# Optimization experiments

Hardware: AMD Instinct MI355X
Metric: run time of the kernel (lower is better)

## Reference

```python
import jax, jax.numpy as jnp
import numpy as np

INPUT_DIM = 512
HIDDEN_DIM = 1024


def glorot_normal(key, shape):
    fan_in, fan_out = shape[0], shape[1]
    std = jnp.sqrt(2.0 / (fan_in + fan_out))
    return std * jax.random.normal(key, shape, dtype=jnp.float32)


def setup_inputs() -> dict:
    key = jax.random.key(0)
    k1, k2, k3 = jax.random.split(key, 3)
    b, t = 32, 1024
    H = HIDDEN_DIM + INPUT_DIM
    x_btd = jax.random.normal(k1, (b, t, INPUT_DIM), dtype=jnp.float32)
    input_paddings = jnp.zeros((b, t), dtype=jnp.float32)
    kernel = glorot_normal(k2, (H, 4 * HIDDEN_DIM))  # [H, 4h]
    bias = jnp.zeros((4 * HIDDEN_DIM,), dtype=jnp.float32)
    h_init = glorot_normal(k3, (1, HIDDEN_DIM))
    return {"x_btd": x_btd, "input_paddings": input_paddings,
            "kernel": kernel, "bias": bias, "h_init": h_init}


def lstm_step(carry, x_bd, kernel, bias):
    h_bh, c_bh = carry
    x_bH = jnp.concatenate([x_bd, h_bh], axis=-1)          # [b, d+h]
    gate_out = jnp.einsum('bH,Hh->bh', x_bH, kernel) + bias  # [b, 4h]
    f, i, o, g = jnp.split(gate_out, 4, axis=-1)
    c_new = jax.nn.sigmoid(f) * c_bh + jax.nn.sigmoid(i) * jnp.tanh(g)
    h_new = jax.nn.sigmoid(o) * jnp.tanh(c_new)
    return (h_new, c_new), h_new


def reference(x_btd, input_paddings, kernel, bias, h_init) -> jnp.ndarray:
    del input_paddings
    b = x_btd.shape[0]
    h0 = jnp.tile(h_init, (b, 1))                # [b, h]
    c0 = jnp.zeros((b, HIDDEN_DIM), dtype=x_btd.dtype)
    x_tbd = jnp.transpose(x_btd, (1, 0, 2))      # [t, b, d]

    def step(carry, x_bd):
        return lstm_step(carry, x_bd, kernel, bias)

    _, h_tbh = jax.lax.scan(step, (h0, c0), x_tbd)
    return jnp.transpose(h_tbh, (1, 0, 2))       # [b, t, h]
```

## Files before the change

kernel.cpp:

```cpp
#include <hip/hip_runtime.h>


#define T_STEPS 1024
#define BATCH   32
#define DIN     512
#define HID     1024
#define KTOT    1536
#define NBLK    128
#define REDSTR  36
#define REDW    (32*REDSTR)
#define NSLOT   8
#define FLAGSTR 16

typedef __attribute__((ext_vector_type(8))) short  short8;
typedef __attribute__((ext_vector_type(4))) float  floatx4;
typedef __attribute__((ext_vector_type(4))) int    intx4;
typedef __attribute__((ext_vector_type(4))) unsigned short ushort4_;

#define MFMA16(a,b,c) __builtin_amdgcn_mfma_f32_16x16x32_bf16(a, b, c, 0, 0, 0)

__device__ __forceinline__ unsigned short f2bf(float f) {
    unsigned u = __builtin_bit_cast(unsigned, f);
    u += 0x7FFFu + ((u >> 16) & 1u);
    return (unsigned short)(u >> 16);
}
__device__ __forceinline__ float sigf(float x) { return 1.f / (1.f + __expf(-x)); }
__device__ __forceinline__ float tanh_fast(float x) {
    float e = __expf(2.f * x);
    return 1.f - 2.f / (e + 1.f);
}

__device__ __forceinline__ floatx4 coh_load16(const void* p) {
    floatx4 v;
    asm volatile("global_load_dwordx4 %0, %1, off sc1" : "=v"(v) : "v"(p));
    return v;
}
__device__ __forceinline__ intx4 coh_load16i(const void* p) {
    intx4 v;
    asm volatile("global_load_dwordx4 %0, %1, off sc1\n\ts_waitcnt vmcnt(0)"
                 : "=v"(v) : "v"(p) : "memory");
    return v;
}
__device__ __forceinline__ void coh_store16(void* p, short8 v) {
    asm volatile("global_store_dwordx4 %0, %1, off sc1" :: "v"(p), "v"(v) : "memory");
}
__device__ __forceinline__ void coh_store4(void* p, int v) {
    asm volatile("global_store_dword %0, %1, off sc1" :: "v"(p), "v"(v) : "memory");
}
__device__ __forceinline__ void wait_vm0() {
    asm volatile("s_waitcnt vmcnt(0)" ::: "memory");
}

__global__ __launch_bounds__(256) void prep_wt(const float* __restrict__ kern,
                                               unsigned short* __restrict__ wt) {
    __shared__ unsigned short tile[64][72];
    const int c0 = (blockIdx.x & 63) * 64;
    const int k0 = (blockIdx.x >> 6) * 64;
    const int cl = threadIdx.x & 63;
    const int kg = threadIdx.x >> 6;
    #pragma unroll
    for (int i = 0; i < 16; ++i) {
        int kl = kg * 16 + i;
        tile[cl][kl] = f2bf(kern[(k0 + kl) * 4096 + c0 + cl]);
    }
    __syncthreads();
    #pragma unroll
    for (int i = 0; i < 16; ++i) {
        int cc = kg * 16 + i;
        wt[(size_t)(c0 + cc) * KTOT + k0 + cl] = tile[cc][cl];
    }
}

__global__ __launch_bounds__(256) void prep_x(const float* __restrict__ x,
                                              unsigned short* __restrict__ xT) {
    const int row = blockIdx.x * 2 + (threadIdx.x >> 7);
    const int l   = threadIdx.x & 127;
    const int b = row >> 10, t = row & 1023;
    float4 v = ((const float4*)(x + (size_t)row * DIN))[l];
    ushort4_ o;
    o.x = f2bf(v.x); o.y = f2bf(v.y); o.z = f2bf(v.z); o.w = f2bf(v.w);
    *(ushort4_*)(xT + ((size_t)t * BATCH + b) * DIN + l * 4) = o;
}

__global__ __launch_bounds__(256) void init_h(const float* __restrict__ h_init,
                                              unsigned short* __restrict__ hbuf,
                                              int* __restrict__ flags) {
    if (blockIdx.x == 32) {
        for (int i = threadIdx.x; i < NBLK * FLAGSTR; i += 256) flags[i] = 0;
        return;
    }
    const int p0 = blockIdx.x * 4;
    const int u = threadIdx.x & 7;
    #pragma unroll
    for (int j = 0; j < 4; ++j) {
        const int p = p0 + j;
        hbuf[p * 256 + threadIdx.x] = f2bf(h_init[p * 8 + u]);
    }
}

__global__ __launch_bounds__(512, 2) void lstm_persist(
    const unsigned short* __restrict__ wt,
    const unsigned short* __restrict__ xT,
    unsigned short* __restrict__ hbuf,
    int* __restrict__ flags,
    const float* __restrict__ bias,
    float* __restrict__ out)
{
    __shared__ float red[NSLOT][REDW];
    __shared__ __align__(16) unsigned short hLDS[256];

    const int bk   = blockIdx.x;
    const int tid  = threadIdx.x;
    const int wave = tid >> 6;
    const int lane = tid & 63;
    const int lrow = lane & 15;
    const int kq   = lane >> 4;
    const bool isG = wave < 4;
    const int  sl  = wave & 3;

    short8 wb[8][2];
    if (isG) {
        #pragma unroll
        for (int i = 0; i < 4; ++i) {
            const int k = sl * 128 + i * 32 + kq * 8;
            #pragma unroll
            for (int c = 0; c < 2; ++c) {
                const int cl = lrow + c * 16;
                const int gcol = (cl >> 3) * HID + bk * 8 + (cl & 7);
                wb[i][c] = *(const short8*)(wt + (size_t)gcol * KTOT + k);
            }
        }
    } else {
        #pragma unroll
        for (int i = 0; i < 8; ++i) {
            const int k = 512 + sl * 256 + i * 32 + kq * 8;
            #pragma unroll
            for (int c = 0; c < 2; ++c) {
                const int cl = lrow + c * 16;
                const int gcol = (cl >> 3) * HID + bk * 8 + (cl & 7);
                wb[i][c] = *(const short8*)(wt + (size_t)gcol * KTOT + k);
            }
        }
    }

    const int pb = tid >> 3;
    const int pu = tid & 7;
    float bias_r[4];
    float c_state = 0.f;
    if (tid < 256) {
        #pragma unroll
        for (int g = 0; g < 4; ++g) bias_r[g] = bias[g * HID + bk * 8 + pu];
    }

    const int* myflag = flags + (sl * 32 + (lane & 31)) * FLAGSTR;

    floatx4 xa[4][2];

    {
        const floatx4 zero = {0.f, 0.f, 0.f, 0.f};
        floatx4 acc[2][2] = {{zero, zero}, {zero, zero}};
        if (isG) {
            const unsigned short* xb = xT;
            #pragma unroll
            for (int i = 0; i < 4; ++i) {
                const int k = sl * 128 + i * 32 + kq * 8;
                short8 a0 = *(const short8*)(xb + lrow * DIN + k);
                short8 a1 = *(const short8*)(xb + (lrow + 16) * DIN + k);
                acc[0][0] = MFMA16(a0, wb[i][0], acc[0][0]);
                acc[0][1] = MFMA16(a0, wb[i][1], acc[0][1]);
                acc[1][0] = MFMA16(a1, wb[i][0], acc[1][0]);
                acc[1][1] = MFMA16(a1, wb[i][1], acc[1][1]);
            }
            const unsigned short* xn = xT + (size_t)1 * (BATCH * DIN);
            #pragma unroll
            for (int i = 0; i < 4; ++i) {
                const int k = sl * 128 + i * 32 + kq * 8;
                xa[i][0] = *(const floatx4*)(xn + lrow * DIN + k);
                xa[i][1] = *(const floatx4*)(xn + (lrow + 16) * DIN + k);
            }
        } else {
            floatx4 ha[8][2];
            #pragma unroll
            for (int i = 0; i < 8; ++i) {
                const int p = sl * 32 + i * 4 + kq;
                ha[i][0] = coh_load16(hbuf + p * 256 + lrow * 8);
                ha[i][1] = coh_load16(hbuf + p * 256 + (lrow + 16) * 8);
            }
            wait_vm0();
            __builtin_amdgcn_sched_barrier(0);
            #pragma unroll
            for (int i = 0; i < 8; ++i) {
                short8 a0 = __builtin_bit_cast(short8, ha[i][0]);
                short8 a1 = __builtin_bit_cast(short8, ha[i][1]);
                acc[0][0] = MFMA16(a0, wb[i][0], acc[0][0]);
                acc[0][1] = MFMA16(a0, wb[i][1], acc[0][1]);
                acc[1][0] = MFMA16(a1, wb[i][0], acc[1][0]);
                acc[1][1] = MFMA16(a1, wb[i][1], acc[1][1]);
            }
        }
        #pragma unroll
        for (int mt = 0; mt < 2; ++mt)
            #pragma unroll
            for (int nt = 0; nt < 2; ++nt)
                #pragma unroll
                for (int r = 0; r < 4; ++r)
                    red[wave][(mt * 16 + kq * 4 + r) * REDSTR + nt * 16 + lrow]
                        = acc[mt][nt][r];
    }

    for (int t = 0; t < T_STEPS; ++t) {
        __syncthreads();

        if (tid < 256) {
            float gv[4];
            #pragma unroll
            for (int g = 0; g < 4; ++g) {
                float s = bias_r[g];
                #pragma unroll
                for (int w = 0; w < NSLOT; ++w)
                    s += red[w][pb * REDSTR + g * 8 + pu];
                gv[g] = s;
            }
            const float fg = sigf(gv[0]);
            const float ig = sigf(gv[1]);
            const float og = sigf(gv[2]);
            const float gg = tanh_fast(gv[3]);
            c_state = fg * c_state + ig * gg;
            const float hn = og * tanh_fast(c_state);

            if (t + 1 < T_STEPS) {
                hLDS[tid] = f2bf(hn);
                asm volatile("s_waitcnt lgkmcnt(0)" ::: "memory");
                if (lane < 8) {
                    short8 v = *(const short8*)(hLDS + wave * 64 + lane * 8);
                    coh_store16(hbuf + (size_t)((t + 1) & 1) * (NBLK * 256)
                                     + bk * 256 + (wave * 8 + lane) * 8, v);
                }
                wait_vm0();
                if (lane == 0)
                    coh_store4(flags + bk * FLAGSTR + wave, t + 1);
            }
            out[(size_t)pb * (T_STEPS * HID) + (size_t)t * HID + bk * 8 + pu] = hn;
        }

        if (t + 1 == T_STEPS) break;

        __syncthreads();

        const floatx4 zero = {0.f, 0.f, 0.f, 0.f};
        floatx4 acc[2][2] = {{zero, zero}, {zero, zero}};
        if (isG) {
            #pragma unroll
            for (int i = 0; i < 4; ++i) {
                short8 a0 = __builtin_bit_cast(short8, xa[i][0]);
                short8 a1 = __builtin_bit_cast(short8, xa[i][1]);
                acc[0][0] = MFMA16(a0, wb[i][0], acc[0][0]);
                acc[0][1] = MFMA16(a0, wb[i][1], acc[0][1]);
                acc[1][0] = MFMA16(a1, wb[i][0], acc[1][0]);
                acc[1][1] = MFMA16(a1, wb[i][1], acc[1][1]);
            }
            if (t + 2 < T_STEPS) {
                const unsigned short* xn = xT + (size_t)(t + 2) * (BATCH * DIN);
                #pragma unroll
                for (int i = 0; i < 4; ++i) {
                    const int k = sl * 128 + i * 32 + kq * 8;
                    xa[i][0] = *(const floatx4*)(xn + lrow * DIN + k);
                    xa[i][1] = *(const floatx4*)(xn + (lrow + 16) * DIN + k);
                }
            }
        } else {
            const int tgt = t + 1;
            while (true) {
                intx4 f = coh_load16i(myflag);
                if (f.x >= tgt && f.y >= tgt && f.z >= tgt && f.w >= tgt) break;
                __builtin_amdgcn_s_sleep(1);
            }
            const unsigned short* hb = hbuf + (size_t)((t + 1) & 1) * (NBLK * 256);
            floatx4 ha[8][2];
            #pragma unroll
            for (int i = 0; i < 8; ++i) {
                const int p = sl * 32 + i * 4 + kq;
                ha[i][0] = coh_load16(hb + p * 256 + lrow * 8);
                ha[i][1] = coh_load16(hb + p * 256 + (lrow + 16) * 8);
            }
            wait_vm0();
            __builtin_amdgcn_sched_barrier(0);
            #pragma unroll
            for (int i = 0; i < 8; ++i) {
                short8 a0 = __builtin_bit_cast(short8, ha[i][0]);
                short8 a1 = __builtin_bit_cast(short8, ha[i][1]);
                acc[0][0] = MFMA16(a0, wb[i][0], acc[0][0]);
                acc[0][1] = MFMA16(a0, wb[i][1], acc[0][1]);
                acc[1][0] = MFMA16(a1, wb[i][0], acc[1][0]);
                acc[1][1] = MFMA16(a1, wb[i][1], acc[1][1]);
            }
        }
        #pragma unroll
        for (int mt = 0; mt < 2; ++mt)
            #pragma unroll
            for (int nt = 0; nt < 2; ++nt)
                #pragma unroll
                for (int r = 0; r < 4; ++r)
                    red[wave][(mt * 16 + kq * 4 + r) * REDSTR + nt * 16 + lrow]
                        = acc[mt][nt][r];
    }
}

extern "C" void kernel_launch(void* const* d_in, const int* in_sizes, int n_in,
                              void* d_out, int out_size, void* d_ws, size_t ws_size,
                              hipStream_t stream) {
    (void)in_sizes; (void)n_in; (void)out_size;
    const float* x      = (const float*)d_in[0];
    const float* kern   = (const float*)d_in[2];
    const float* bias   = (const float*)d_in[3];
    const float* h_init = (const float*)d_in[4];
    float* out = (float*)d_out;

    char* ws = (char*)d_ws;
    unsigned short* wt    = (unsigned short*)(ws);
    unsigned short* xT    = (unsigned short*)(ws + 12582912);
    unsigned short* hbuf  = (unsigned short*)(ws + 12582912 + 33554432);
    int*            flags = (int*)(ws + 12582912 + 33554432 + 131072);
    (void)ws_size;

    prep_wt<<<dim3(64 * 24), dim3(256), 0, stream>>>(kern, wt);
    prep_x<<<dim3(BATCH * T_STEPS / 2), dim3(256), 0, stream>>>(x, xT);
    init_h<<<dim3(33), dim3(256), 0, stream>>>(h_init, hbuf, flags);

    void* args[] = { &wt, &xT, &hbuf, &flags, &bias, &out };
    hipLaunchCooperativeKernel((const void*)lstm_persist, dim3(NBLK), dim3(512),
                               args, 0, stream);
}
```

Before: 4.401 ms.

## Embed step-parity tag in fp32 hidden state to replace flag polling

The separate per-block flag array and its store-then-flag-store handshake are removed. Each hidden value is now written as fp32 with its low mantissa bit replaced by a step-parity tag, and consumers poll the data itself until every tag matches, then convert to bf16 with v_cvt_pk_bf16_f32. The x-projection MFMAs are also moved into the gate waves' post-activation phase so they overlap with the h polling, dropping one barrier-separated segment. The cost is doubled hidden-state traffic (fp32 instead of bf16), wider polling reads, and one mantissa bit of precision lost in h.

```diff
diff --git a/kernel.cpp b/kernel.cpp
--- a/kernel.cpp
+++ b/kernel.cpp
@@ -10,11 +10,11 @@
 #define REDSTR  36
 #define REDW    (32*REDSTR)
 #define NSLOT   8
-#define FLAGSTR 16
+#define HSLOT   (NBLK*256)
 
 typedef __attribute__((ext_vector_type(8))) short  short8;
 typedef __attribute__((ext_vector_type(4))) float  floatx4;
-typedef __attribute__((ext_vector_type(4))) int    intx4;
+typedef __attribute__((ext_vector_type(4))) unsigned int uintx4;
 typedef __attribute__((ext_vector_type(4))) unsigned short ushort4_;
 
 #define MFMA16(a,b,c) __builtin_amdgcn_mfma_f32_16x16x32_bf16(a, b, c, 0, 0, 0)
@@ -29,22 +29,18 @@
     float e = __expf(2.f * x);
     return 1.f - 2.f / (e + 1.f);
 }
-
-__device__ __forceinline__ floatx4 coh_load16(const void* p) {
+__device__ __forceinline__ unsigned cvt2(float a, float b) {
+    unsigned r;
+    asm("v_cvt_pk_bf16_f32 %0, %1, %2" : "=v"(r) : "v"(a), "v"(b));
+    return r;
+}
+
+__device__ __forceinline__ floatx4 coh_load16f(const void* p) {
     floatx4 v;
     asm volatile("global_load_dwordx4 %0, %1, off sc1" : "=v"(v) : "v"(p));
     return v;
 }
-__device__ __forceinline__ intx4 coh_load16i(const void* p) {
-    intx4 v;
-    asm volatile("global_load_dwordx4 %0, %1, off sc1\n\ts_waitcnt vmcnt(0)"
-                 : "=v"(v) : "v"(p) : "memory");
-    return v;
-}
-__device__ __forceinline__ void coh_store16(void* p, short8 v) {
-    asm volatile("global_store_dwordx4 %0, %1, off sc1" :: "v"(p), "v"(v) : "memory");
-}
-__device__ __forceinline__ void coh_store4(void* p, int v) {
+__device__ __forceinline__ void coh_store4u(void* p, unsigned v) {
     asm volatile("global_store_dword %0, %1, off sc1" :: "v"(p), "v"(v) : "memory");
 }
 __device__ __forceinline__ void wait_vm0() {
@@ -83,31 +79,26 @@
 }
 
 __global__ __launch_bounds__(256) void init_h(const float* __restrict__ h_init,
-                                              unsigned short* __restrict__ hbuf,
-                                              int* __restrict__ flags) {
-    if (blockIdx.x == 32) {
-        for (int i = threadIdx.x; i < NBLK * FLAGSTR; i += 256) flags[i] = 0;
-        return;
-    }
+                                              unsigned* __restrict__ hbuf_u) {
     const int p0 = blockIdx.x * 4;
     const int u = threadIdx.x & 7;
     #pragma unroll
     for (int j = 0; j < 4; ++j) {
         const int p = p0 + j;
-        hbuf[p * 256 + threadIdx.x] = f2bf(h_init[p * 8 + u]);
+        unsigned tv = __builtin_bit_cast(unsigned, h_init[p * 8 + u]) & ~1u;
+        hbuf_u[p * 256 + threadIdx.x] = tv;
+        hbuf_u[HSLOT + p * 256 + threadIdx.x] = 1u;
     }
 }
 
 __global__ __launch_bounds__(512, 2) void lstm_persist(
     const unsigned short* __restrict__ wt,
     const unsigned short* __restrict__ xT,
-    unsigned short* __restrict__ hbuf,
-    int* __restrict__ flags,
+    float* __restrict__ hbuf,
     const float* __restrict__ bias,
     float* __restrict__ out)
 {
     __shared__ float red[NSLOT][REDW];
-    __shared__ __align__(16) unsigned short hLDS[256];
 
     const int bk   = blockIdx.x;
     const int tid  = threadIdx.x;
@@ -118,6 +109,8 @@
     const bool isG = wave < 4;
     const int  sl  = wave & 3;
 
+    unsigned* hbuf_u = (unsigned*)hbuf;
+
     short8 wb[8][2];
     if (isG) {
         #pragma unroll
@@ -151,8 +144,6 @@
         #pragma unroll
         for (int g = 0; g < 4; ++g) bias_r[g] = bias[g * HID + bk * 8 + pu];
     }
-
-    const int* myflag = flags + (sl * 32 + (lane & 31)) * FLAGSTR;
 
     floatx4 xa[4][2];
 
@@ -179,23 +170,33 @@
                 xa[i][1] = *(const floatx4*)(xn + (lrow + 16) * DIN + k);
             }
         } else {
-            floatx4 ha[8][2];
+            floatx4 hf[8][2][2];
             #pragma unroll
             for (int i = 0; i < 8; ++i) {
                 const int p = sl * 32 + i * 4 + kq;
-                ha[i][0] = coh_load16(hbuf + p * 256 + lrow * 8);
-                ha[i][1] = coh_load16(hbuf + p * 256 + (lrow + 16) * 8);
+                #pragma unroll
+                for (int c = 0; c < 2; ++c) {
+                    const float* src = hbuf + p * 256 + (lrow + c * 16) * 8;
+                    hf[i][c][0] = coh_load16f(src);
+                    hf[i][c][1] = coh_load16f(src + 4);
+                }
             }
             wait_vm0();
             __builtin_amdgcn_sched_barrier(0);
             #pragma unroll
             for (int i = 0; i < 8; ++i) {
-                short8 a0 = __builtin_bit_cast(short8, ha[i][0]);
-                short8 a1 = __builtin_bit_cast(short8, ha[i][1]);
-                acc[0][0] = MFMA16(a0, wb[i][0], acc[0][0]);
-                acc[0][1] = MFMA16(a0, wb[i][1], acc[0][1]);
-                acc[1][0] = MFMA16(a1, wb[i][0], acc[1][0]);
-                acc[1][1] = MFMA16(a1, wb[i][1], acc[1][1]);
+                union { short8 s; unsigned u[4]; } wa[2];
+                #pragma unroll
+                for (int c = 0; c < 2; ++c) {
+                    wa[c].u[0] = cvt2(hf[i][c][0][0], hf[i][c][0][1]);
+                    wa[c].u[1] = cvt2(hf[i][c][0][2], hf[i][c][0][3]);
+                    wa[c].u[2] = cvt2(hf[i][c][1][0], hf[i][c][1][1]);
+                    wa[c].u[3] = cvt2(hf[i][c][1][2], hf[i][c][1][3]);
+                }
+                acc[0][0] = MFMA16(wa[0].s, wb[i][0], acc[0][0]);
+                acc[0][1] = MFMA16(wa[0].s, wb[i][1], acc[0][1]);
+                acc[1][0] = MFMA16(wa[1].s, wb[i][0], acc[1][0]);
+                acc[1][1] = MFMA16(wa[1].s, wb[i][1], acc[1][1]);
             }
         }
         #pragma unroll
@@ -210,6 +211,12 @@
 
     for (int t = 0; t < T_STEPS; ++t) {
         __syncthreads();
+
+        const unsigned tg = ((unsigned)(t + 1) >> 1) & 1u;
+        const size_t   so = (size_t)((t + 1) & 1) * HSLOT;
+
+        const floatx4 zero = {0.f, 0.f, 0.f, 0.f};
+        floatx4 acc[2][2] = {{zero, zero}, {zero, zero}};
 
         if (tid < 256) {
             float gv[4];
@@ -229,72 +236,81 @@
             const float hn = og * tanh_fast(c_state);
 
             if (t + 1 < T_STEPS) {
-                hLDS[tid] = f2bf(hn);
-                asm volatile("s_waitcnt lgkmcnt(0)" ::: "memory");
-                if (lane < 8) {
-                    short8 v = *(const short8*)(hLDS + wave * 64 + lane * 8);
-                    coh_store16(hbuf + (size_t)((t + 1) & 1) * (NBLK * 256)
-                                     + bk * 256 + (wave * 8 + lane) * 8, v);
+                unsigned hv = (__builtin_bit_cast(unsigned, hn) & ~1u) | tg;
+                coh_store4u(hbuf_u + so + bk * 256 + tid, hv);
+            }
+            out[(size_t)pb * (T_STEPS * HID) + (size_t)t * HID + bk * 8 + pu] = hn;
+
+            if (t + 1 < T_STEPS) {
+                #pragma unroll
+                for (int i = 0; i < 4; ++i) {
+                    short8 a0 = __builtin_bit_cast(short8, xa[i][0]);
+                    short8 a1 = __builtin_bit_cast(short8, xa[i][1]);
+                    acc[0][0] = MFMA16(a0, wb[i][0], acc[0][0]);
+                    acc[0][1] = MFMA16(a0, wb[i][1], acc[0][1]);
+                    acc[1][0] = MFMA16(a1, wb[i][0], acc[1][0]);
+                    acc[1][1] = MFMA16(a1, wb[i][1], acc[1][1]);
+                }
+                if (t + 2 < T_STEPS) {
+                    const unsigned short* xn = xT + (size_t)(t + 2) * (BATCH * DIN);
+                    #pragma unroll
+                    for (int i = 0; i < 4; ++i) {
+                        const int k = sl * 128 + i * 32 + kq * 8;
+                        xa[i][0] = *(const floatx4*)(xn + lrow * DIN + k);
+                        xa[i][1] = *(const floatx4*)(xn + (lrow + 16) * DIN + k);
+                    }
+                }
+            }
+        } else if (t + 1 < T_STEPS) {
+            const float* hb = hbuf + so;
+            floatx4 hf[8][2][2];
+            while (true) {
+                #pragma unroll
+                for (int i = 0; i < 8; ++i) {
+                    const int p = sl * 32 + i * 4 + kq;
+                    #pragma unroll
+                    for (int c = 0; c < 2; ++c) {
+                        const float* src = hb + p * 256 + (lrow + c * 16) * 8;
+                        hf[i][c][0] = coh_load16f(src);
+                        hf[i][c][1] = coh_load16f(src + 4);
+                    }
                 }
                 wait_vm0();
-                if (lane == 0)
-                    coh_store4(flags + bk * FLAGSTR + wave, t + 1);
-            }
-            out[(size_t)pb * (T_STEPS * HID) + (size_t)t * HID + bk * 8 + pu] = hn;
+                __builtin_amdgcn_sched_barrier(0);
+                unsigned od = 0;
+                #pragma unroll
+                for (int i = 0; i < 8; ++i)
+                    #pragma unroll
+                    for (int c = 0; c < 2; ++c)
+                        #pragma unroll
+                        for (int h2 = 0; h2 < 2; ++h2) {
+                            uintx4 u = __builtin_bit_cast(uintx4, hf[i][c][h2]);
+                            od |= u[0] ^ tg; od |= u[1] ^ tg;
+                            od |= u[2] ^ tg; od |= u[3] ^ tg;
+                        }
+                if (!__any((int)(od & 1u))) break;
+                __builtin_amdgcn_s_sleep(1);
+            }
+            #pragma unroll
+            for (int i = 0; i < 8; ++i) {
+                union { short8 s; unsigned u[4]; } wa[2];
+                #pragma unroll
+                for (int c = 0; c < 2; ++c) {
+                    wa[c].u[0] = cvt2(hf[i][c][0][0], hf[i][c][0][1]);
+                    wa[c].u[1] = cvt2(hf[i][c][0][2], hf[i][c][0][3]);
+                    wa[c].u[2] = cvt2(hf[i][c][1][0], hf[i][c][1][1]);
+                    wa[c].u[3] = cvt2(hf[i][c][1][2], hf[i][c][1][3]);
+                }
+                acc[0][0] = MFMA16(wa[0].s, wb[i][0], acc[0][0]);
+                acc[0][1] = MFMA16(wa[0].s, wb[i][1], acc[0][1]);
+                acc[1][0] = MFMA16(wa[1].s, wb[i][0], acc[1][0]);
+                acc[1][1] = MFMA16(wa[1].s, wb[i][1], acc[1][1]);
+            }
         }
 
         if (t + 1 == T_STEPS) break;
-
         __syncthreads();
 
-        const floatx4 zero = {0.f, 0.f, 0.f, 0.f};
-        floatx4 acc[2][2] = {{zero, zero}, {zero, zero}};
-        if (isG) {
-            #pragma unroll
-            for (int i = 0; i < 4; ++i) {
-                short8 a0 = __builtin_bit_cast(short8, xa[i][0]);
-                short8 a1 = __builtin_bit_cast(short8, xa[i][1]);
-                acc[0][0] = MFMA16(a0, wb[i][0], acc[0][0]);
-                acc[0][1] = MFMA16(a0, wb[i][1], acc[0][1]);
-                acc[1][0] = MFMA16(a1, wb[i][0], acc[1][0]);
-                acc[1][1] = MFMA16(a1, wb[i][1], acc[1][1]);
-            }
-            if (t + 2 < T_STEPS) {
-                const unsigned short* xn = xT + (size_t)(t + 2) * (BATCH * DIN);
-                #pragma unroll
-                for (int i = 0; i < 4; ++i) {
-                    const int k = sl * 128 + i * 32 + kq * 8;
-                    xa[i][0] = *(const floatx4*)(xn + lrow * DIN + k);
-                    xa[i][1] = *(const floatx4*)(xn + (lrow + 16) * DIN + k);
-                }
-            }
-        } else {
-            const int tgt = t + 1;
-            while (true) {
-                intx4 f = coh_load16i(myflag);
-                if (f.x >= tgt && f.y >= tgt && f.z >= tgt && f.w >= tgt) break;
-                __builtin_amdgcn_s_sleep(1);
-            }
-            const unsigned short* hb = hbuf + (size_t)((t + 1) & 1) * (NBLK * 256);
-            floatx4 ha[8][2];
-            #pragma unroll
-            for (int i = 0; i < 8; ++i) {
-                const int p = sl * 32 + i * 4 + kq;
-                ha[i][0] = coh_load16(hb + p * 256 + lrow * 8);
-                ha[i][1] = coh_load16(hb + p * 256 + (lrow + 16) * 8);
-            }
-            wait_vm0();
-            __builtin_amdgcn_sched_barrier(0);
-            #pragma unroll
-            for (int i = 0; i < 8; ++i) {
-                short8 a0 = __builtin_bit_cast(short8, ha[i][0]);
-                short8 a1 = __builtin_bit_cast(short8, ha[i][1]);
-                acc[0][0] = MFMA16(a0, wb[i][0], acc[0][0]);
-                acc[0][1] = MFMA16(a0, wb[i][1], acc[0][1]);
-                acc[1][0] = MFMA16(a1, wb[i][0], acc[1][0]);
-                acc[1][1] = MFMA16(a1, wb[i][1], acc[1][1]);
-            }
-        }
         #pragma unroll
         for (int mt = 0; mt < 2; ++mt)
             #pragma unroll
@@ -317,17 +333,16 @@
     float* out = (float*)d_out;
 
     char* ws = (char*)d_ws;
-    unsigned short* wt    = (unsigned short*)(ws);
-    unsigned short* xT    = (unsigned short*)(ws + 12582912);
-    unsigned short* hbuf  = (unsigned short*)(ws + 12582912 + 33554432);
-    int*            flags = (int*)(ws + 12582912 + 33554432 + 131072);
+    unsigned short* wt   = (unsigned short*)(ws);
+    unsigned short* xT   = (unsigned short*)(ws + 12582912);
+    float*          hbuf = (float*)(ws + 12582912 + 33554432);
     (void)ws_size;
 
     prep_wt<<<dim3(64 * 24), dim3(256), 0, stream>>>(kern, wt);
     prep_x<<<dim3(BATCH * T_STEPS / 2), dim3(256), 0, stream>>>(x, xT);
-    init_h<<<dim3(33), dim3(256), 0, stream>>>(h_init, hbuf, flags);
-
-    void* args[] = { &wt, &xT, &hbuf, &flags, &bias, &out };
+    init_h<<<dim3(32), dim3(256), 0, stream>>>(h_init, (unsigned*)hbuf);
+
+    void* args[] = { &wt, &xT, &hbuf, &bias, &out };
     hipLaunchCooperativeKernel((const void*)lstm_persist, dim3(NBLK), dim3(512),
                                args, 0, stream);
 }
```

Result: slower. 7.637 ms (+73.5%).
